# Kernel tuning notes

Measured on AMD Instinct MI355X. Metric: run time of the kernel, lower is better.

Reference implementation:

```python
import jax, jax.numpy as jnp
import numpy as np

B, N, S, K, D = 8, 16384, 1024, 32, 64
MLP = [64, 64, 128]
C_IN = 3 + D  # grouped_xyz_norm (3) concat grouped point features (D)
EPS = 1e-5


def setup_inputs() -> dict:
    key = jax.random.key(0)
    ks = jax.random.split(key, 16)
    inp = {
        "xyz": jax.random.normal(ks[0], (B, 3, N), dtype=jnp.float32),
        "points": jax.random.normal(ks[1], (B, D, N), dtype=jnp.float32),
        "sample_idx": jax.random.randint(ks[2], (B, S), 0, N, dtype=jnp.int32),
    }
    last = C_IN
    for i, oc in enumerate(MLP):
        scale = 1.0 / np.sqrt(last)
        inp[f"w{i}"] = jax.random.uniform(ks[3 + 4 * i], (oc, last), jnp.float32, -scale, scale)
        inp[f"b{i}"] = jax.random.uniform(ks[4 + 4 * i], (oc,), jnp.float32, -scale, scale)
        inp[f"g{i}"] = jnp.ones((oc,), jnp.float32)   # BN gamma
        inp[f"be{i}"] = jnp.zeros((oc,), jnp.float32)  # BN beta
        last = oc
    return inp


def _gather(pts, idx):
    # pts: [B,N,C], idx: [B,...] -> [B,...,C]
    return jax.vmap(lambda p, i: p[i])(pts, idx)


def _mlp_layer(x, w, b, g, be):
    # x: [B,C,K,S]; 1x1 Conv2d + BatchNorm2d (training-mode batch stats) + ReLU
    y = jnp.einsum("bcks,oc->boks", x, w) + b[None, :, None, None]
    mu = jnp.mean(y, axis=(0, 2, 3), keepdims=True)
    var = jnp.var(y, axis=(0, 2, 3), keepdims=True)
    y = (y - mu) * jax.lax.rsqrt(var + EPS)
    y = y * g[None, :, None, None] + be[None, :, None, None]
    return jax.nn.relu(y)


def reference(xyz, points, sample_idx, w0, b0, g0, be0, w1, b1, g1, be1, w2, b2, g2, be2):
    xyz_t = jnp.transpose(xyz, (0, 2, 1))      # [B,N,3]
    pts_t = jnp.transpose(points, (0, 2, 1))   # [B,N,D]
    idx_s = sample_idx.astype(jnp.int32)

    new_xyz = _gather(xyz_t, idx_s)            # [B,S,3]

    # square_distance(new_xyz, xyz): [B,S,N]
    d = (jnp.sum(new_xyz ** 2, -1)[:, :, None]
         + jnp.sum(xyz_t ** 2, -1)[:, None, :]
         - 2.0 * jnp.einsum("bsc,bnc->bsn", new_xyz, xyz_t))
    _, idx = jax.lax.top_k(-d, K)              # kNN indices [B,S,K]

    grouped_xyz = _gather(xyz_t, idx)          # [B,S,K,3]
    grouped_norm = grouped_xyz - new_xyz[:, :, None, :]
    grouped_pts = _gather(pts_t, idx)          # [B,S,K,D]
    feat = jnp.concatenate([grouped_norm, grouped_pts], axis=-1)  # [B,S,K,3+D]

    x = jnp.transpose(feat, (0, 3, 2, 1))      # [B,C,K,S]
    x = _mlp_layer(x, w0, b0, g0, be0)
    x = _mlp_layer(x, w1, b1, g1, be1)
    x = _mlp_layer(x, w2, b2, g2, be2)
    new_points = jnp.max(x, axis=2)            # [B,128,S]

    return (jnp.transpose(new_xyz, (0, 2, 1)), new_points, grouped_xyz, idx_s)
```

## Files before the change

### kernel.cpp

```cpp
#include <hip/hip_runtime.h>

constexpr int cB = 8, cN = 16384, cS = 1024, cK = 32, cD = 64;
constexpr int cO2 = 128;
constexpr int PTOT = cB * cS * cK;
constexpr int NBLK2 = PTOT / 128;

constexpr int OUT1_OFF = cB * 3 * cS;
constexpr int OUT2_OFF = OUT1_OFF + cB * cO2 * cS;
constexpr int OUT3_OFF = OUT2_OFF + cB * cS * cK * 3;

constexpr size_t WS_PTS  = 0;
constexpr size_t WS_XYZP = WS_PTS  + (size_t)cB * cN * cD * 4;
constexpr size_t WS_IDX  = WS_XYZP + (size_t)cB * cN * 16;
constexpr size_t WS_NORM = WS_IDX  + (size_t)PTOT * 4;
constexpr size_t WS_Y0   = WS_NORM + (size_t)PTOT * 3 * 4;
constexpr size_t WS_Y1   = WS_Y0   + (size_t)PTOT * 64 * 4;
constexpr size_t WS_MX   = WS_Y1   + (size_t)PTOT * 64 * 4;
constexpr size_t WS_MN   = WS_MX   + (size_t)cB * cS * cO2 * 4;
constexpr size_t WS_P0   = WS_MN   + (size_t)cB * cS * cO2 * 4;
constexpr size_t WS_P1   = WS_P0   + (size_t)NBLK2 * 64 * 2 * 8;
constexpr size_t WS_P2   = WS_P1   + (size_t)NBLK2 * 64 * 2 * 8;
constexpr size_t WS_BN   = WS_P2   + (size_t)NBLK2 * 128 * 2 * 8;
constexpr size_t WS_END  = WS_BN   + 3 * 128 * 2 * 4;

__device__ __forceinline__ unsigned keyOf(float d) {
    unsigned u = __float_as_uint(d);
    return u ^ ((unsigned)((int)u >> 31) | 0x80000000u);
}
__device__ __forceinline__ float distNp(float qx, float qy, float qz, float sq, float4 p) {
    float m0 = __fmul_rn(qx, p.x);
    float m1 = __fmul_rn(qy, p.y);
    float m2 = __fmul_rn(qz, p.z);
    float dt = __fadd_rn(__fadd_rn(m0, m1), m2);
    return __fsub_rn(__fadd_rn(sq, p.w), __fmul_rn(2.0f, dt));
}

__global__ __launch_bounds__(256) void k_prep(const float* __restrict__ pts,
                                              const float* __restrict__ xyz,
                                              float* __restrict__ ptsT,
                                              float4* __restrict__ xyzp) {
    __shared__ float tile[64][65];
    int blk = blockIdx.x;
    int tid = threadIdx.x;
    if (blk < 2048) {
        int b = blk >> 8;
        int n0 = (blk & 255) * 64;
        for (int it = 0; it < 16; ++it) {
            int l = it * 256 + tid;
            int c = l >> 6, nn = l & 63;
            tile[nn][c] = pts[((size_t)b * 64 + c) * cN + n0 + nn];
        }
        __syncthreads();
        for (int it = 0; it < 16; ++it) {
            int l = it * 256 + tid;
            int nn = l >> 6, c = l & 63;
            ptsT[((size_t)(b * cN + n0 + nn)) * 64 + c] = tile[nn][c];
        }
    } else {
        int i = (blk - 2048) * 256 + tid;
        int b = i >> 14, n = i & (cN - 1);
        float x = xyz[(b * 3 + 0) * cN + n];
        float y = xyz[(b * 3 + 1) * cN + n];
        float z = xyz[(b * 3 + 2) * cN + n];
        float sq = __fadd_rn(__fadd_rn(__fmul_rn(x, x), __fmul_rn(y, y)), __fmul_rn(z, z));
        xyzp[i] = make_float4(x, y, z, sq);
    }
}

#define QB 8
#define CAP2 192

__device__ __forceinline__ void selectBin2(const unsigned* __restrict__ h, int lane,
                                           int target, int* Tout, int* cbOut) {
    int base = lane * 8;
    unsigned hh[8];
    unsigned c8 = 0;
#pragma unroll
    for (int i = 0; i < 8; i++) { hh[i] = h[base + i]; c8 += hh[i]; }
    unsigned incl = c8;
#pragma unroll
    for (int off = 1; off < 32; off <<= 1) {
        unsigned t = __shfl_up(incl, (unsigned)off, 32);
        if (lane >= off) incl += t;
    }
    int excl = (int)(incl - c8);
    if (excl < target && target <= (int)incl) {
        int c = excl;
#pragma unroll
        for (int i = 0; i < 8; i++) {
            int nc = c + (int)hh[i];
            if (c < target && target <= nc) { *Tout = base + i; *cbOut = c; }
            c = nc;
        }
    }
}

__global__ __launch_bounds__(256, 4) void k_knn(const float* __restrict__ xyz,
                                                const int* __restrict__ sidx_g,
                                                const float4* __restrict__ xyzp,
                                                int* __restrict__ idxw,
                                                float* __restrict__ normw,
                                                float* __restrict__ outbuf) {
    __shared__ unsigned hist[QB][258];
    __shared__ unsigned long long wmask[QB][256];
    __shared__ unsigned long long cand2[QB][CAP2];
    __shared__ unsigned cnt2[QB];
    __shared__ float qxs[QB], qys[QB], qzs[QB], sqs[QB];
    __shared__ int sIdx[QB];
    __shared__ float s1s[QB], tAs[QB], tBs[QB];
    __shared__ int T1s[QB], cb1s[QB], T2s[QB], cb2s[QB];
    __shared__ float fTs[QB];
    __shared__ int nRf[QB];
    __shared__ int anyR;
    __shared__ unsigned order[QB][cK];

    int tid = threadIdx.x;
    int qi = tid >> 5, lane = tid & 31;
    int wid = tid >> 6;
    int qbase = blockIdx.x * QB;
    int b = qbase / cS;
    int s0 = qbase % cS;
    const float4* pb = xyzp + (size_t)b * cN;

    if (tid < QB) {
        int si = sidx_g[b * cS + s0 + tid];
        sIdx[tid] = si;
        float x = xyz[(b * 3 + 0) * cN + si];
        float y = xyz[(b * 3 + 1) * cN + si];
        float z = xyz[(b * 3 + 2) * cN + si];
        qxs[tid] = x; qys[tid] = y; qzs[tid] = z;
        sqs[tid] = __fadd_rn(__fadd_rn(__fmul_rn(x, x), __fmul_rn(y, y)), __fmul_rn(z, z));
        cnt2[tid] = 0u;
    }
    if (tid == 0) anyR = 0;
    for (int i = tid; i < QB * 258; i += 256) ((unsigned*)hist)[i] = 0u;
    __syncthreads();

    float qx = qxs[qi], qy = qys[qi], qz = qzs[qi], qsq = sqs[qi];

    {
        float dmin = 3.4e38f;
        for (int t = 0; t < 64; ++t) {
            float4 p = pb[lane + 32 * t];
            float dot = fmaf(qx, p.x, fmaf(qy, p.y, qz * p.z));
            float d = fmaf(-2.0f, dot, qsq + p.w);
            dmin = fminf(dmin, d);
        }
        float rmax = dmin;
#pragma unroll
        for (int off = 16; off; off >>= 1)
            rmax = fmaxf(rmax, __shfl_xor(rmax, off, 32));
        if (lane == 0) {
            float R = fmaxf(rmax, 1e-12f);
            float s1 = 254.0f / R;
            s1s[qi] = s1;
            tAs[qi] = qsq * s1;
            tBs[qi] = -2.0f * s1;
        }
    }
    __syncthreads();

    float lqx[QB], lqy[QB], lqz[QB], lS[QB], lA[QB], lB[QB];
#pragma unroll
    for (int q = 0; q < QB; q++) {
        lqx[q] = qxs[q]; lqy[q] = qys[q]; lqz[q] = qzs[q];
        lS[q] = s1s[q]; lA[q] = tAs[q]; lB[q] = tBs[q];
    }
    bool wlead = (tid & 63) == 0;

    for (int j = 0; j < cN / 256; ++j) {
        float4 p = pb[j * 256 + tid];
#pragma unroll
        for (int q = 0; q < QB; ++q) {
            float dot = fmaf(lqx[q], p.x, fmaf(lqy[q], p.y, lqz[q] * p.z));
            float t = fmaf(dot, lB[q], fmaf(p.w, lS[q], lA[q]));
            unsigned long long mk = __ballot(t < 258.0f);
            if (wlead) wmask[q][j * 4 + wid] = mk;
            if (t < 258.0f) {
                int bin = __float2int_rz(fmaxf(t, 0.0f));
                atomicAdd(&hist[q][bin], 1u);
            }
        }
    }
    __syncthreads();

    selectBin2(hist[qi], lane, cK, &T1s[qi], &cb1s[qi]);
    __syncthreads();
    if (tid < QB) {
        int T1 = T1s[tid];
        int acc = cb1s[tid] + (int)hist[tid][T1] + (int)hist[tid][T1 + 1];
        int nr = (acc > CAP2) ? 1 : 0;
        nRf[tid] = nr;
        fTs[tid] = (float)(T1 + 2);
        if (nr) atomicOr(&anyR, 1);
    }
    __syncthreads();

    if (anyR) {
        for (int i = tid; i < QB * 258; i += 256) ((unsigned*)hist)[i] = 0u;
        __syncthreads();
        if (nRf[qi]) {
            float fT1 = (float)T1s[qi];
            float tB = tBs[qi], tS = s1s[qi], tA = tAs[qi];
            for (int w = lane; w < 256; w += 32) {
                unsigned long long m = wmask[qi][w];
                int base = w * 64;
                while (m) {
                    int bit = (int)__ffsll((unsigned long long)m) - 1;
                    m &= m - 1;
                    float4 p = pb[base + bit];
                    float dot = fmaf(qx, p.x, fmaf(qy, p.y, qz * p.z));
                    float t = fmaf(dot, tB, fmaf(p.w, tS, tA));
                    float um = fmaxf(t, 0.0f) - fT1;
                    if (um >= 0.0f && um < 2.0f)
                        atomicAdd(&hist[qi][min(255, __float2int_rz(um * 128.0f))], 1u);
                }
            }
        }
        __syncthreads();
        if (nRf[qi]) selectBin2(hist[qi], lane, cK - cb1s[qi], &T2s[qi], &cb2s[qi]);
        __syncthreads();
        if (tid < QB && nRf[tid])
            fTs[tid] = (float)T1s[tid] + (float)(T2s[tid] + 2) * 0.0078125f;
        __syncthreads();
    }

    {
        float fT = fTs[qi];
        float tB = tBs[qi], tS = s1s[qi], tA = tAs[qi];
        for (int w = lane; w < 256; w += 32) {
            unsigned long long m = wmask[qi][w];
            int base = w * 64;
            while (m) {
                int bit = (int)__ffsll((unsigned long long)m) - 1;
                m &= m - 1;
                int n = base + bit;
                float4 p = pb[n];
                float dot = fmaf(qx, p.x, fmaf(qy, p.y, qz * p.z));
                float t = fmaf(dot, tB, fmaf(p.w, tS, tA));
                if (t < fT) {
                    float de = distNp(qx, qy, qz, qsq, p);
                    unsigned pos = atomicAdd(&cnt2[qi], 1u);
                    if (pos < CAP2)
                        cand2[qi][pos] = ((unsigned long long)keyOf(de) << 32) | (unsigned)n;
                }
            }
        }
    }
    __syncthreads();

    int m2 = (int)min(cnt2[qi], (unsigned)CAP2);
    for (int r = 0; r < cK; ++r) {
        unsigned long long best = ~0ull;
        int bslot = -1;
        for (int i = lane; i < m2; i += 32) {
            unsigned long long v = cand2[qi][i];
            if (v < best) { best = v; bslot = i; }
        }
#pragma unroll
        for (int off = 16; off; off >>= 1) {
            unsigned long long ov = __shfl_xor(best, off, 32);
            int os = __shfl_xor(bslot, off, 32);
            if (ov < best) { best = ov; bslot = os; }
        }
        if (lane == 0) {
            order[qi][r] = (best != ~0ull) ? (unsigned)(best & 0xFFFFFFFFull) : 0u;
            if (bslot >= 0) cand2[qi][bslot] = ~0ull;
        }
    }

    {
        int r = lane;
        int s = s0 + qi;
        int n = (int)order[qi][r];
        size_t pos = (size_t)(b * cS + s) * cK + r;
        idxw[pos] = n;
        float px = xyz[(b * 3 + 0) * cN + n];
        float py = xyz[(b * 3 + 1) * cN + n];
        float pz = xyz[(b * 3 + 2) * cN + n];
        outbuf[OUT2_OFF + pos * 3 + 0] = px;
        outbuf[OUT2_OFF + pos * 3 + 1] = py;
        outbuf[OUT2_OFF + pos * 3 + 2] = pz;
        normw[pos * 3 + 0] = __fsub_rn(px, qxs[qi]);
        normw[pos * 3 + 1] = __fsub_rn(py, qys[qi]);
        normw[pos * 3 + 2] = __fsub_rn(pz, qzs[qi]);
        if (r == 0) {
            outbuf[OUT3_OFF + b * cS + s] = (float)sIdx[qi];
            outbuf[(b * 3 + 0) * cS + s] = qxs[qi];
            outbuf[(b * 3 + 1) * cS + s] = qys[qi];
            outbuf[(b * 3 + 2) * cS + s] = qzs[qi];
        }
    }
}

__global__ __launch_bounds__(256) void k_conv0(const int* __restrict__ idxw,
                                               const float* __restrict__ normw,
                                               const float* __restrict__ ptsT,
                                               const float* __restrict__ w0,
                                               const float* __restrict__ b0,
                                               float* __restrict__ y0,
                                               double* __restrict__ part0) {
    __shared__ __align__(16) float fAT[67 * 132];
    __shared__ __align__(16) float wT[67 * 68];
    __shared__ float bl[64];
    int tid = threadIdx.x;
    int blk = blockIdx.x;
    int b = blk >> 8;
    int s0 = (blk & 255) << 2;
    size_t posbase = ((size_t)b * cS + s0) * cK;

    for (int l = tid; l < 64 * 67; l += 256) {
        int o = l / 67, c = l - o * 67;
        wT[c * 68 + o] = w0[l];
    }
    if (tid < 64) bl[tid] = b0[tid];
    {
        int r = tid >> 1, half = tid & 1;
        size_t pos = posbase + r;
        int n = idxw[pos];
        const float* pr = ptsT + ((size_t)b * cN + n) * 64 + half * 32;
#pragma unroll
        for (int q = 0; q < 8; q++) {
            float4 v = *(const float4*)(pr + q * 4);
            int c = 3 + half * 32 + q * 4;
            fAT[(c + 0) * 132 + r] = v.x;
            fAT[(c + 1) * 132 + r] = v.y;
            fAT[(c + 2) * 132 + r] = v.z;
            fAT[(c + 3) * 132 + r] = v.w;
        }
        if (half == 0) {
            fAT[0 * 132 + r] = normw[pos * 3 + 0];
            fAT[1 * 132 + r] = normw[pos * 3 + 1];
            fAT[2 * 132 + r] = normw[pos * 3 + 2];
        }
    }
    __syncthreads();

    int ry = tid >> 4, tx = tid & 15;
    float acc[8][4];
#pragma unroll
    for (int i = 0; i < 8; i++)
#pragma unroll
        for (int j = 0; j < 4; j++) acc[i][j] = bl[tx * 4 + j];

    for (int c = 0; c < 67; ++c) {
        const float* fb = fAT + c * 132;
        float4 a0 = *(const float4*)(fb + ry * 8);
        float4 a1 = *(const float4*)(fb + ry * 8 + 4);
        float4 wv = *(const float4*)&wT[c * 68 + tx * 4];
        float av[8] = {a0.x, a0.y, a0.z, a0.w, a1.x, a1.y, a1.z, a1.w};
#pragma unroll
        for (int i = 0; i < 8; i++) {
            acc[i][0] = fmaf(av[i], wv.x, acc[i][0]);
            acc[i][1] = fmaf(av[i], wv.y, acc[i][1]);
            acc[i][2] = fmaf(av[i], wv.z, acc[i][2]);
            acc[i][3] = fmaf(av[i], wv.w, acc[i][3]);
        }
    }
#pragma unroll
    for (int i = 0; i < 8; i++) {
        float4 o4 = make_float4(acc[i][0], acc[i][1], acc[i][2], acc[i][3]);
        *(float4*)(y0 + (posbase + ry * 8 + i) * 64 + tx * 4) = o4;
    }
    __syncthreads();

    float* ps = wT;
    float* pq = wT + 16 * 64;
#pragma unroll
    for (int j = 0; j < 4; j++) {
        float s = 0.f, q = 0.f;
#pragma unroll
        for (int i = 0; i < 8; i++) { float v = acc[i][j]; s += v; q += v * v; }
        ps[ry * 64 + tx * 4 + j] = s;
        pq[ry * 64 + tx * 4 + j] = q;
    }
    __syncthreads();
    if (tid < 64) {
        float s = 0.f, q = 0.f;
        for (int t = 0; t < 16; t++) { s += ps[t * 64 + tid]; q += pq[t * 64 + tid]; }
        part0[((size_t)blk * 64 + tid) * 2 + 0] = (double)s;
        part0[((size_t)blk * 64 + tid) * 2 + 1] = (double)q;
    }
}

__global__ __launch_bounds__(256) void k_conv1(const float* __restrict__ yin,
                                               const float2* __restrict__ bnin,
                                               const float* __restrict__ w,
                                               const float* __restrict__ bb,
                                               float* __restrict__ yout,
                                               double* __restrict__ part) {
    __shared__ __align__(16) float fAT[64 * 132];
    __shared__ __align__(16) float wT[64 * 68];
    __shared__ float bl[64], al[64], sl[64];
    int tid = threadIdx.x;
    int blk = blockIdx.x;
    int b = blk >> 8;
    int s0 = (blk & 255) << 2;
    size_t posbase = ((size_t)b * cS + s0) * cK;

    if (tid < 64) {
        bl[tid] = bb[tid];
        float2 t = bnin[tid];
        al[tid] = t.x; sl[tid] = t.y;
    }
    __syncthreads();
    for (int l = tid; l < 64 * 64; l += 256) {
        int o = l >> 6, c = l & 63;
        wT[c * 68 + o] = w[l];
    }
    {
        int r = tid >> 1, half = tid & 1;
        const float* yr = yin + (posbase + r) * 64 + half * 32;
#pragma unroll
        for (int q = 0; q < 8; q++) {
            float4 v = *(const float4*)(yr + q * 4);
            int c = half * 32 + q * 4;
            v.x = fmaxf(fmaf(v.x, al[c + 0], sl[c + 0]), 0.0f);
            v.y = fmaxf(fmaf(v.y, al[c + 1], sl[c + 1]), 0.0f);
            v.z = fmaxf(fmaf(v.z, al[c + 2], sl[c + 2]), 0.0f);
            v.w = fmaxf(fmaf(v.w, al[c + 3], sl[c + 3]), 0.0f);
            fAT[(c + 0) * 132 + r] = v.x;
            fAT[(c + 1) * 132 + r] = v.y;
            fAT[(c + 2) * 132 + r] = v.z;
            fAT[(c + 3) * 132 + r] = v.w;
        }
    }
    __syncthreads();

    int ry = tid >> 4, tx = tid & 15;
    float acc[8][4];
#pragma unroll
    for (int i = 0; i < 8; i++)
#pragma unroll
        for (int j = 0; j < 4; j++) acc[i][j] = bl[tx * 4 + j];

    for (int c = 0; c < 64; ++c) {
        const float* fb = fAT + c * 132;
        float4 a0 = *(const float4*)(fb + ry * 8);
        float4 a1 = *(const float4*)(fb + ry * 8 + 4);
        float4 wv = *(const float4*)&wT[c * 68 + tx * 4];
        float av[8] = {a0.x, a0.y, a0.z, a0.w, a1.x, a1.y, a1.z, a1.w};
#pragma unroll
        for (int i = 0; i < 8; i++) {
            acc[i][0] = fmaf(av[i], wv.x, acc[i][0]);
            acc[i][1] = fmaf(av[i], wv.y, acc[i][1]);
            acc[i][2] = fmaf(av[i], wv.z, acc[i][2]);
            acc[i][3] = fmaf(av[i], wv.w, acc[i][3]);
        }
    }
#pragma unroll
    for (int i = 0; i < 8; i++) {
        float4 o4 = make_float4(acc[i][0], acc[i][1], acc[i][2], acc[i][3]);
        *(float4*)(yout + (posbase + ry * 8 + i) * 64 + tx * 4) = o4;
    }
    __syncthreads();

    float* ps = wT;
    float* pq = wT + 16 * 64;
#pragma unroll
    for (int j = 0; j < 4; j++) {
        float s = 0.f, q = 0.f;
#pragma unroll
        for (int i = 0; i < 8; i++) { float v = acc[i][j]; s += v; q += v * v; }
        ps[ry * 64 + tx * 4 + j] = s;
        pq[ry * 64 + tx * 4 + j] = q;
    }
    __syncthreads();
    if (tid < 64) {
        float s = 0.f, q = 0.f;
        for (int t = 0; t < 16; t++) { s += ps[t * 64 + tid]; q += pq[t * 64 + tid]; }
        part[((size_t)blk * 64 + tid) * 2 + 0] = (double)s;
        part[((size_t)blk * 64 + tid) * 2 + 1] = (double)q;
    }
}

__global__ __launch_bounds__(256) void k_conv2(const float* __restrict__ y1,
                                               const float2* __restrict__ bn1,
                                               const float* __restrict__ w2,
                                               const float* __restrict__ b2,
                                               float* __restrict__ mx,
                                               float* __restrict__ mn,
                                               double* __restrict__ part2) {
    __shared__ __align__(16) float fAT[64 * 132];
    __shared__ __align__(16) float wT[64 * 132];
    __shared__ float al[64], sl[64], bl[128];
    int tid = threadIdx.x;
    int blk = blockIdx.x;
    int b = blk >> 8;
    int s0 = (blk & 255) << 2;
    size_t posbase = ((size_t)b * cS + s0) * cK;

    if (tid < 64) { float2 t = bn1[tid]; al[tid] = t.x; sl[tid] = t.y; }
    if (tid < 128) bl[tid] = b2[tid];
    __syncthreads();

    {
        int r = tid >> 1, half = tid & 1;
        const float* yr = y1 + (posbase + r) * 64 + half * 32;
#pragma unroll
        for (int q = 0; q < 8; q++) {
            float4 v = *(const float4*)(yr + q * 4);
            int c = half * 32 + q * 4;
            v.x = fmaxf(fmaf(v.x, al[c + 0], sl[c + 0]), 0.0f);
            v.y = fmaxf(fmaf(v.y, al[c + 1], sl[c + 1]), 0.0f);
            v.z = fmaxf(fmaf(v.z, al[c + 2], sl[c + 2]), 0.0f);
            v.w = fmaxf(fmaf(v.w, al[c + 3], sl[c + 3]), 0.0f);
            fAT[(c + 0) * 132 + r] = v.x;
            fAT[(c + 1) * 132 + r] = v.y;
            fAT[(c + 2) * 132 + r] = v.z;
            fAT[(c + 3) * 132 + r] = v.w;
        }
    }
    for (int l = tid; l < 128 * 64; l += 256) {
        int o = l >> 6, c = l & 63;
        wT[c * 132 + o] = w2[l];
    }
    __syncthreads();

    int ry = tid >> 4, tx = tid & 15;
    float acc[8][8];
#pragma unroll
    for (int i = 0; i < 8; i++) {
#pragma unroll
        for (int j = 0; j < 4; j++) acc[i][j] = bl[tx * 4 + j];
#pragma unroll
        for (int j = 4; j < 8; j++) acc[i][j] = bl[64 + tx * 4 + (j - 4)];
    }

    for (int c = 0; c < 64; ++c) {
        const float* fb = fAT + c * 132;
        const float* wb = wT + c * 132;
        float4 a0 = *(const float4*)(fb + ry * 8);
        float4 a1 = *(const float4*)(fb + ry * 8 + 4);
        float4 w0v = *(const float4*)(wb + tx * 4);
        float4 w1v = *(const float4*)(wb + 64 + tx * 4);
        float av[8] = {a0.x, a0.y, a0.z, a0.w, a1.x, a1.y, a1.z, a1.w};
        float wv[8] = {w0v.x, w0v.y, w0v.z, w0v.w, w1v.x, w1v.y, w1v.z, w1v.w};
#pragma unroll
        for (int i = 0; i < 8; i++)
#pragma unroll
            for (int j = 0; j < 8; j++)
                acc[i][j] = fmaf(av[i], wv[j], acc[i][j]);
    }
    __syncthreads();

    float* ps  = wT;
    float* pq  = wT + 16 * 128;
    float* pmx = wT + 32 * 128;
    float* pmn = wT + 48 * 128;
#pragma unroll
    for (int j = 0; j < 8; j++) {
        int o = (j < 4) ? (tx * 4 + j) : (64 + tx * 4 + (j - 4));
        float s = 0.f, q = 0.f;
        float mv = -3.402823466e+38f, nv = 3.402823466e+38f;
#pragma unroll
        for (int i = 0; i < 8; i++) {
            float v = acc[i][j];
            s += v; q += v * v;
            mv = fmaxf(mv, v); nv = fminf(nv, v);
        }
        ps[ry * 128 + o] = s;
        pq[ry * 128 + o] = q;
        pmx[ry * 128 + o] = mv;
        pmn[ry * 128 + o] = nv;
    }
    __syncthreads();
    if (tid < 128) {
        float s = 0.f, q = 0.f;
        for (int t = 0; t < 16; t++) { s += ps[t * 128 + tid]; q += pq[t * 128 + tid]; }
        part2[((size_t)blk * 128 + tid) * 2 + 0] = (double)s;
        part2[((size_t)blk * 128 + tid) * 2 + 1] = (double)q;
    }
    for (int e = tid; e < 512; e += 256) {
        int sg = e >> 7, o = e & 127;
        float mv = -3.402823466e+38f, nv = 3.402823466e+38f;
        for (int t = sg * 4; t < sg * 4 + 4; ++t) {
            mv = fmaxf(mv, pmx[t * 128 + o]);
            nv = fminf(nv, pmn[t * 128 + o]);
        }
        int s = s0 + sg;
        mx[((size_t)b * cS + s) * 128 + o] = mv;
        mn[((size_t)b * cS + s) * 128 + o] = nv;
    }
}

__global__ __launch_bounds__(256) void k_fin(const double* __restrict__ part, int nblk,
                                             int oc,
                                             const float* __restrict__ g,
                                             const float* __restrict__ be,
                                             float2* __restrict__ bnout) {
    __shared__ double rs[256], rq[256];
    int o = blockIdx.x;
    int tid = threadIdx.x;
    double s = 0.0, q = 0.0;
    for (int i = tid; i < nblk; i += 256) {
        const double* p = part + ((size_t)i * oc + o) * 2;
        s += p[0];
        q += p[1];
    }
    rs[tid] = s; rq[tid] = q;
    __syncthreads();
    for (int off = 128; off; off >>= 1) {
        if (tid < off) { rs[tid] += rs[tid + off]; rq[tid] += rq[tid + off]; }
        __syncthreads();
    }
    if (tid == 0) {
        double cntv = (double)PTOT;
        double mu = rs[0] / cntv;
        double var = rq[0] / cntv - mu * mu;
        if (var < 0.0) var = 0.0;
        float a = (float)((double)g[o] / sqrt(var + 1e-5));
        float sh = (float)((double)be[o] - mu * (double)a);
        bnout[o] = make_float2(a, sh);
    }
}

__global__ __launch_bounds__(256) void k_final(const float* __restrict__ mx,
                                               const float* __restrict__ mn,
                                               const float2* __restrict__ bn2,
                                               float* __restrict__ out1) {
    int i = blockIdx.x * 256 + threadIdx.x;
    int b = i >> 17;
    int r = i & ((1 << 17) - 1);
    int o = r >> 10;
    int s = r & 1023;
    float2 t = bn2[o];
    size_t idx = ((size_t)b * cS + s) * 128 + o;
    float M = (t.x >= 0.0f) ? mx[idx] : mn[idx];
    out1[i] = fmaxf(t.x * M + t.y, 0.0f);
}

extern "C" void kernel_launch(void* const* d_in, const int* in_sizes, int n_in,
                              void* d_out, int out_size, void* d_ws, size_t ws_size,
                              hipStream_t stream) {
    (void)in_sizes; (void)n_in; (void)out_size;
    const float* xyz = (const float*)d_in[0];
    const float* pts = (const float*)d_in[1];
    const int* sidx  = (const int*)d_in[2];
    const float* w0  = (const float*)d_in[3];
    const float* b0  = (const float*)d_in[4];
    const float* g0  = (const float*)d_in[5];
    const float* be0 = (const float*)d_in[6];
    const float* w1  = (const float*)d_in[7];
    const float* b1  = (const float*)d_in[8];
    const float* g1  = (const float*)d_in[9];
    const float* be1 = (const float*)d_in[10];
    const float* w2  = (const float*)d_in[11];
    const float* b2  = (const float*)d_in[12];
    const float* g2  = (const float*)d_in[13];
    const float* be2 = (const float*)d_in[14];
    float* out = (float*)d_out;
    char* ws = (char*)d_ws;
    if (ws_size < WS_END) return;

    float* ptsT  = (float*)(ws + WS_PTS);
    float4* xyzp = (float4*)(ws + WS_XYZP);
    int* idxw    = (int*)(ws + WS_IDX);
    float* normw = (float*)(ws + WS_NORM);
    float* y0    = (float*)(ws + WS_Y0);
    float* y1    = (float*)(ws + WS_Y1);
    float* mx    = (float*)(ws + WS_MX);
    float* mn    = (float*)(ws + WS_MN);
    double* p0   = (double*)(ws + WS_P0);
    double* p1   = (double*)(ws + WS_P1);
    double* p2   = (double*)(ws + WS_P2);
    float2* bnb  = (float2*)(ws + WS_BN);

    hipLaunchKernelGGL(k_prep, dim3(2048 + cB * cN / 256), dim3(256), 0, stream,
                       pts, xyz, ptsT, xyzp);
    hipLaunchKernelGGL(k_knn, dim3(cB * cS / QB), dim3(256), 0, stream,
                       xyz, sidx, xyzp, idxw, normw, out);
    hipLaunchKernelGGL(k_conv0, dim3(NBLK2), dim3(256), 0, stream,
                       idxw, normw, ptsT, w0, b0, y0, p0);
    hipLaunchKernelGGL(k_fin, dim3(64), dim3(256), 0, stream, p0, NBLK2, 64, g0, be0, bnb);
    hipLaunchKernelGGL(k_conv1, dim3(NBLK2), dim3(256), 0, stream, y0, bnb, w1, b1, y1, p1);
    hipLaunchKernelGGL(k_fin, dim3(64), dim3(256), 0, stream, p1, NBLK2, 64, g1, be1, bnb + 128);
    hipLaunchKernelGGL(k_conv2, dim3(NBLK2), dim3(256), 0, stream,
                       y1, bnb + 128, w2, b2, mx, mn, p2);
    hipLaunchKernelGGL(k_fin, dim3(128), dim3(256), 0, stream, p2, NBLK2, 128, g2, be2, bnb + 256);
    hipLaunchKernelGGL(k_final, dim3(cB * cO2 * cS / 256), dim3(256), 0, stream,
                       mx, mn, bnb + 256, out + OUT1_OFF);
}
```

Measured before the change: 395.9 us.

## Bin points into a 2D spatial grid and scan only nearby cells in kNN

Adds counting, scan and scatter kernels that sort the points of each batch into a 32x32 grid over (z,y) and reorder the queries along a serpentine cell order, so the eight queries in a block are spatially close. The kNN kernel then computes a bounding window of cells from each query's radius estimate and runs its histogram, refine and candidate passes only over points in those cells, instead of the full 16K points and the wavefront ballot masks. This cuts distance work and drops the wmask shared buffer. In exchange it adds several small launches and atomics, and it relies on the fixed grid range of ±4.5, beyond which coordinates are clamped into the edge cells.

```diff
diff --git a/kernel.cpp b/kernel.cpp
--- a/kernel.cpp
+++ b/kernel.cpp
@@ -4,6 +4,11 @@
 constexpr int cO2 = 128;
 constexpr int PTOT = cB * cS * cK;
 constexpr int NBLK2 = PTOT / 128;
+
+constexpr int GR = 32;
+constexpr int GC2 = GR * GR;
+#define GL 4.5f
+#define GINV (32.0f / 9.0f)
 
 constexpr int OUT1_OFF = cB * 3 * cS;
 constexpr int OUT2_OFF = OUT1_OFF + cB * cO2 * cS;
@@ -23,6 +28,13 @@
 constexpr size_t WS_BN   = WS_P2   + (size_t)NBLK2 * 128 * 2 * 8;
 constexpr size_t WS_END  = WS_BN   + 3 * 128 * 2 * 4;
 
+constexpr size_t WS_SPT  = WS_Y0;
+constexpr size_t WS_SIX  = WS_SPT + (size_t)cB * cN * 16;
+constexpr size_t WS_PCNT = WS_SIX + (size_t)cB * cN * 4;
+constexpr size_t WS_QCNT = WS_PCNT + (size_t)cB * GC2 * 4;
+constexpr size_t WS_PCS  = WS_QCNT + (size_t)cB * GC2 * 4;
+constexpr size_t WS_QORD = WS_PCS + (size_t)cB * (GC2 + 1) * 4;
+
 __device__ __forceinline__ unsigned keyOf(float d) {
     unsigned u = __float_as_uint(d);
     return u ^ ((unsigned)((int)u >> 31) | 0x80000000u);
@@ -33,6 +45,18 @@
     float m2 = __fmul_rn(qz, p.z);
     float dt = __fadd_rn(__fadd_rn(m0, m1), m2);
     return __fsub_rn(__fadd_rn(sq, p.w), __fmul_rn(2.0f, dt));
+}
+
+__device__ __forceinline__ int cellClamp(float v) {
+    return min(GR - 1, max(0, (int)floorf((v + GL) * GINV)));
+}
+__device__ __forceinline__ int pcell(float4 p) {
+    return cellClamp(p.z) * GR + cellClamp(p.y);
+}
+__device__ __forceinline__ int qkey(float qy, float qz) {
+    int cy = cellClamp(qy), cz = cellClamp(qz);
+    int yy = (cz & 1) ? (GR - 1 - cy) : cy;
+    return cz * GR + yy;
 }
 
 __global__ __launch_bounds__(256) void k_prep(const float* __restrict__ pts,
@@ -67,6 +91,82 @@
     }
 }
 
+__global__ __launch_bounds__(256) void k_cnt(const float4* __restrict__ xyzp,
+                                             const float* __restrict__ xyz,
+                                             const int* __restrict__ sidx_g,
+                                             int* __restrict__ pcnt,
+                                             int* __restrict__ qcnt) {
+    int blk = blockIdx.x, tid = threadIdx.x;
+    if (blk < 512) {
+        int i = blk * 256 + tid;
+        int b = i >> 14;
+        atomicAdd(&pcnt[b * GC2 + pcell(xyzp[i])], 1);
+    } else {
+        int i = (blk - 512) * 256 + tid;
+        int b = i >> 10, s = i & (cS - 1);
+        int si = sidx_g[b * cS + s];
+        float qy = xyz[(b * 3 + 1) * cN + si];
+        float qz = xyz[(b * 3 + 2) * cN + si];
+        atomicAdd(&qcnt[b * GC2 + qkey(qy, qz)], 1);
+    }
+}
+
+__global__ __launch_bounds__(256) void k_scan(int* __restrict__ pcnt,
+                                              int* __restrict__ qcnt,
+                                              int* __restrict__ pcs) {
+    __shared__ int s[256];
+    int b = blockIdx.x >> 1, kind = blockIdx.x & 1;
+    int tid = threadIdx.x;
+    int* cnt = (kind == 0) ? (pcnt + b * GC2) : (qcnt + b * GC2);
+    const int CBC = GC2 / 256;
+    int base = tid * CBC;
+    int sum = 0;
+    for (int k = 0; k < CBC; ++k) sum += cnt[base + k];
+    s[tid] = sum;
+    __syncthreads();
+    for (int off = 1; off < 256; off <<= 1) {
+        int v = (tid >= off) ? s[tid - off] : 0;
+        __syncthreads();
+        s[tid] += v;
+        __syncthreads();
+    }
+    int run = s[tid] - sum;
+    for (int k = 0; k < CBC; ++k) {
+        int v = cnt[base + k];
+        if (kind == 0) pcs[(size_t)b * (GC2 + 1) + base + k] = run;
+        cnt[base + k] = run;
+        run += v;
+    }
+    if (kind == 0 && tid == 255) pcs[(size_t)b * (GC2 + 1) + GC2] = run;
+}
+
+__global__ __launch_bounds__(256) void k_scat(const float4* __restrict__ xyzp,
+                                              const float* __restrict__ xyz,
+                                              const int* __restrict__ sidx_g,
+                                              int* __restrict__ pcnt,
+                                              int* __restrict__ qcnt,
+                                              float4* __restrict__ spt,
+                                              int* __restrict__ six,
+                                              int* __restrict__ qord) {
+    int blk = blockIdx.x, tid = threadIdx.x;
+    if (blk < 512) {
+        int i = blk * 256 + tid;
+        int b = i >> 14, n = i & (cN - 1);
+        float4 p = xyzp[i];
+        int pos = atomicAdd(&pcnt[b * GC2 + pcell(p)], 1);
+        spt[(size_t)b * cN + pos] = p;
+        six[(size_t)b * cN + pos] = n;
+    } else {
+        int i = (blk - 512) * 256 + tid;
+        int b = i >> 10, s = i & (cS - 1);
+        int si = sidx_g[b * cS + s];
+        float qy = xyz[(b * 3 + 1) * cN + si];
+        float qz = xyz[(b * 3 + 2) * cN + si];
+        int pos = atomicAdd(&qcnt[b * GC2 + qkey(qy, qz)], 1);
+        qord[b * cS + pos] = s;
+    }
+}
+
 #define QB 8
 #define CAP2 192
 
@@ -98,32 +198,41 @@
 __global__ __launch_bounds__(256, 4) void k_knn(const float* __restrict__ xyz,
                                                 const int* __restrict__ sidx_g,
                                                 const float4* __restrict__ xyzp,
+                                                const float4* __restrict__ spt,
+                                                const int* __restrict__ six,
+                                                const int* __restrict__ pcs,
+                                                const int* __restrict__ qord,
                                                 int* __restrict__ idxw,
                                                 float* __restrict__ normw,
                                                 float* __restrict__ outbuf) {
     __shared__ unsigned hist[QB][258];
-    __shared__ unsigned long long wmask[QB][256];
     __shared__ unsigned long long cand2[QB][CAP2];
     __shared__ unsigned cnt2[QB];
     __shared__ float qxs[QB], qys[QB], qzs[QB], sqs[QB];
-    __shared__ int sIdx[QB];
+    __shared__ int sIdx[QB], sQ[QB];
     __shared__ float s1s[QB], tAs[QB], tBs[QB];
     __shared__ int T1s[QB], cb1s[QB], T2s[QB], cb2s[QB];
     __shared__ float fTs[QB];
     __shared__ int nRf[QB];
     __shared__ int anyR;
+    __shared__ int wzl, wzh, wyl, wyh;
     __shared__ unsigned order[QB][cK];
 
     int tid = threadIdx.x;
     int qi = tid >> 5, lane = tid & 31;
-    int wid = tid >> 6;
     int qbase = blockIdx.x * QB;
     int b = qbase / cS;
     int s0 = qbase % cS;
     const float4* pb = xyzp + (size_t)b * cN;
-
+    const float4* sp = spt + (size_t)b * cN;
+    const int* sx = six + (size_t)b * cN;
+    const int* CSb = pcs + (size_t)b * (GC2 + 1);
+
+    if (tid == 0) { anyR = 0; wzl = GR; wzh = -1; wyl = GR; wyh = -1; }
     if (tid < QB) {
-        int si = sidx_g[b * cS + s0 + tid];
+        int sq = qord[b * cS + s0 + tid];
+        sQ[tid] = sq;
+        int si = sidx_g[b * cS + sq];
         sIdx[tid] = si;
         float x = xyz[(b * 3 + 0) * cN + si];
         float y = xyz[(b * 3 + 1) * cN + si];
@@ -132,7 +241,6 @@
         sqs[tid] = __fadd_rn(__fadd_rn(__fmul_rn(x, x), __fmul_rn(y, y)), __fmul_rn(z, z));
         cnt2[tid] = 0u;
     }
-    if (tid == 0) anyR = 0;
     for (int i = tid; i < QB * 258; i += 256) ((unsigned*)hist)[i] = 0u;
     __syncthreads();
 
@@ -156,6 +264,13 @@
             s1s[qi] = s1;
             tAs[qi] = qsq * s1;
             tBs[qi] = -2.0f * s1;
+            float rq = sqrtf(R * 1.001f);
+            int zlo = max(0, (int)floorf((qz - rq + GL) * GINV));
+            int zhi = min(GR - 1, (int)floorf((qz + rq + GL) * GINV));
+            int ylo = max(0, (int)floorf((qy - rq + GL) * GINV));
+            int yhi = min(GR - 1, (int)floorf((qy + rq + GL) * GINV));
+            atomicMin(&wzl, zlo); atomicMax(&wzh, zhi);
+            atomicMin(&wyl, ylo); atomicMax(&wyh, yhi);
         }
     }
     __syncthreads();
@@ -166,19 +281,20 @@
         lqx[q] = qxs[q]; lqy[q] = qys[q]; lqz[q] = qzs[q];
         lS[q] = s1s[q]; lA[q] = tAs[q]; lB[q] = tBs[q];
     }
-    bool wlead = (tid & 63) == 0;
-
-    for (int j = 0; j < cN / 256; ++j) {
-        float4 p = pb[j * 256 + tid];
-#pragma unroll
-        for (int q = 0; q < QB; ++q) {
-            float dot = fmaf(lqx[q], p.x, fmaf(lqy[q], p.y, lqz[q] * p.z));
-            float t = fmaf(dot, lB[q], fmaf(p.w, lS[q], lA[q]));
-            unsigned long long mk = __ballot(t < 258.0f);
-            if (wlead) wmask[q][j * 4 + wid] = mk;
-            if (t < 258.0f) {
-                int bin = __float2int_rz(fmaxf(t, 0.0f));
-                atomicAdd(&hist[q][bin], 1u);
+    int zl = wzl, zh = wzh, yl = wyl, yh = wyh;
+
+    for (int cz = zl; cz <= zh; ++cz) {
+        int st = CSb[cz * GR + yl], en = CSb[cz * GR + yh + 1];
+        for (int i = st + tid; i < en; i += 256) {
+            float4 p = sp[i];
+#pragma unroll
+            for (int q = 0; q < QB; ++q) {
+                float dot = fmaf(lqx[q], p.x, fmaf(lqy[q], p.y, lqz[q] * p.z));
+                float t = fmaf(dot, lB[q], fmaf(p.w, lS[q], lA[q]));
+                if (t < 258.0f) {
+                    int bin = __float2int_rz(fmaxf(t, 0.0f));
+                    atomicAdd(&hist[q][bin], 1u);
+                }
             }
         }
     }
@@ -199,21 +315,22 @@
     if (anyR) {
         for (int i = tid; i < QB * 258; i += 256) ((unsigned*)hist)[i] = 0u;
         __syncthreads();
-        if (nRf[qi]) {
-            float fT1 = (float)T1s[qi];
-            float tB = tBs[qi], tS = s1s[qi], tA = tAs[qi];
-            for (int w = lane; w < 256; w += 32) {
-                unsigned long long m = wmask[qi][w];
-                int base = w * 64;
-                while (m) {
-                    int bit = (int)__ffsll((unsigned long long)m) - 1;
-                    m &= m - 1;
-                    float4 p = pb[base + bit];
-                    float dot = fmaf(qx, p.x, fmaf(qy, p.y, qz * p.z));
-                    float t = fmaf(dot, tB, fmaf(p.w, tS, tA));
-                    float um = fmaxf(t, 0.0f) - fT1;
-                    if (um >= 0.0f && um < 2.0f)
-                        atomicAdd(&hist[qi][min(255, __float2int_rz(um * 128.0f))], 1u);
+        int lT1[QB], go[QB];
+#pragma unroll
+        for (int q = 0; q < QB; q++) { lT1[q] = T1s[q]; go[q] = nRf[q]; }
+        for (int cz = zl; cz <= zh; ++cz) {
+            int st = CSb[cz * GR + yl], en = CSb[cz * GR + yh + 1];
+            for (int i = st + tid; i < en; i += 256) {
+                float4 p = sp[i];
+#pragma unroll
+                for (int q = 0; q < QB; ++q) {
+                    if (go[q]) {
+                        float dot = fmaf(lqx[q], p.x, fmaf(lqy[q], p.y, lqz[q] * p.z));
+                        float t = fmaf(dot, lB[q], fmaf(p.w, lS[q], lA[q]));
+                        float um = fmaxf(t, 0.0f) - (float)lT1[q];
+                        if (um >= 0.0f && um < 2.0f)
+                            atomicAdd(&hist[q][min(255, __float2int_rz(um * 128.0f))], 1u);
+                    }
                 }
             }
         }
@@ -225,24 +342,24 @@
         __syncthreads();
     }
 
-    {
-        float fT = fTs[qi];
-        float tB = tBs[qi], tS = s1s[qi], tA = tAs[qi];
-        for (int w = lane; w < 256; w += 32) {
-            unsigned long long m = wmask[qi][w];
-            int base = w * 64;
-            while (m) {
-                int bit = (int)__ffsll((unsigned long long)m) - 1;
-                m &= m - 1;
-                int n = base + bit;
-                float4 p = pb[n];
-                float dot = fmaf(qx, p.x, fmaf(qy, p.y, qz * p.z));
-                float t = fmaf(dot, tB, fmaf(p.w, tS, tA));
-                if (t < fT) {
-                    float de = distNp(qx, qy, qz, qsq, p);
-                    unsigned pos = atomicAdd(&cnt2[qi], 1u);
+    float lsq[QB], lt[QB];
+#pragma unroll
+    for (int q = 0; q < QB; q++) { lsq[q] = sqs[q]; lt[q] = fTs[q]; }
+
+    for (int cz = zl; cz <= zh; ++cz) {
+        int st = CSb[cz * GR + yl], en = CSb[cz * GR + yh + 1];
+        for (int i = st + tid; i < en; i += 256) {
+            float4 p = sp[i];
+#pragma unroll
+            for (int q = 0; q < QB; ++q) {
+                float dot = fmaf(lqx[q], p.x, fmaf(lqy[q], p.y, lqz[q] * p.z));
+                float t = fmaf(dot, lB[q], fmaf(p.w, lS[q], lA[q]));
+                if (t < lt[q]) {
+                    float de = distNp(lqx[q], lqy[q], lqz[q], lsq[q], p);
+                    int n = sx[i];
+                    unsigned pos = atomicAdd(&cnt2[q], 1u);
                     if (pos < CAP2)
-                        cand2[qi][pos] = ((unsigned long long)keyOf(de) << 32) | (unsigned)n;
+                        cand2[q][pos] = ((unsigned long long)keyOf(de) << 32) | (unsigned)n;
                 }
             }
         }
@@ -271,7 +388,7 @@
 
     {
         int r = lane;
-        int s = s0 + qi;
+        int s = sQ[qi];
         int n = (int)order[qi][r];
         size_t pos = (size_t)(b * cS + s) * cK + r;
         idxw[pos] = n;
@@ -665,11 +782,23 @@
     double* p1   = (double*)(ws + WS_P1);
     double* p2   = (double*)(ws + WS_P2);
     float2* bnb  = (float2*)(ws + WS_BN);
+    float4* spt  = (float4*)(ws + WS_SPT);
+    int* six     = (int*)(ws + WS_SIX);
+    int* pcnt    = (int*)(ws + WS_PCNT);
+    int* qcnt    = (int*)(ws + WS_QCNT);
+    int* pcs     = (int*)(ws + WS_PCS);
+    int* qord    = (int*)(ws + WS_QORD);
 
     hipLaunchKernelGGL(k_prep, dim3(2048 + cB * cN / 256), dim3(256), 0, stream,
                        pts, xyz, ptsT, xyzp);
+    hipMemsetAsync(ws + WS_PCNT, 0, (size_t)cB * GC2 * 4 * 2, stream);
+    hipLaunchKernelGGL(k_cnt, dim3(512 + 32), dim3(256), 0, stream,
+                       xyzp, xyz, sidx, pcnt, qcnt);
+    hipLaunchKernelGGL(k_scan, dim3(2 * cB), dim3(256), 0, stream, pcnt, qcnt, pcs);
+    hipLaunchKernelGGL(k_scat, dim3(512 + 32), dim3(256), 0, stream,
+                       xyzp, xyz, sidx, pcnt, qcnt, spt, six, qord);
     hipLaunchKernelGGL(k_knn, dim3(cB * cS / QB), dim3(256), 0, stream,
-                       xyz, sidx, xyzp, idxw, normw, out);
+                       xyz, sidx, xyzp, spt, six, pcs, qord, idxw, normw, out);
     hipLaunchKernelGGL(k_conv0, dim3(NBLK2), dim3(256), 0, stream,
                        idxw, normw, ptsT, w0, b0, y0, p0);
     hipLaunchKernelGGL(k_fin, dim3(64), dim3(256), 0, stream, p0, NBLK2, 64, g0, be0, bnb);
```

New measurement: 419.5 us. 1.06x slower.

## Replace ballot-mask candidate compaction in kNN with full rescans; store BN partials as float2

Applied to the files above, without the earlier changes.

The kNN kernel no longer records per-wave ballot masks of points under the histogram threshold. The refinement histogram and candidate collection passes now rescan all N points for every query. This removes the 16KB wmask shared array and the per-iteration ballots, and raises the candidate capacity to 256. In exchange it repeats distance evaluation over every point, and it halves the BN partial-sum traffic by storing float pairs instead of doubles, at some precision risk in the per-block sums.

```diff
diff --git a/kernel.cpp b/kernel.cpp
--- a/kernel.cpp
+++ b/kernel.cpp
@@ -18,9 +18,9 @@
 constexpr size_t WS_MX   = WS_Y1   + (size_t)PTOT * 64 * 4;
 constexpr size_t WS_MN   = WS_MX   + (size_t)cB * cS * cO2 * 4;
 constexpr size_t WS_P0   = WS_MN   + (size_t)cB * cS * cO2 * 4;
-constexpr size_t WS_P1   = WS_P0   + (size_t)NBLK2 * 64 * 2 * 8;
-constexpr size_t WS_P2   = WS_P1   + (size_t)NBLK2 * 64 * 2 * 8;
-constexpr size_t WS_BN   = WS_P2   + (size_t)NBLK2 * 128 * 2 * 8;
+constexpr size_t WS_P1   = WS_P0   + (size_t)NBLK2 * 64 * 8;
+constexpr size_t WS_P2   = WS_P1   + (size_t)NBLK2 * 64 * 8;
+constexpr size_t WS_BN   = WS_P2   + (size_t)NBLK2 * 128 * 8;
 constexpr size_t WS_END  = WS_BN   + 3 * 128 * 2 * 4;
 
 __device__ __forceinline__ unsigned keyOf(float d) {
@@ -68,7 +68,7 @@
 }
 
 #define QB 8
-#define CAP2 192
+#define CAP 256
 
 __device__ __forceinline__ void selectBin2(const unsigned* __restrict__ h, int lane,
                                            int target, int* Tout, int* cbOut) {
@@ -102,21 +102,19 @@
                                                 float* __restrict__ normw,
                                                 float* __restrict__ outbuf) {
     __shared__ unsigned hist[QB][258];
-    __shared__ unsigned long long wmask[QB][256];
-    __shared__ unsigned long long cand2[QB][CAP2];
-    __shared__ unsigned cnt2[QB];
+    __shared__ unsigned long long cand[QB][CAP];
+    __shared__ unsigned cnt[QB];
     __shared__ float qxs[QB], qys[QB], qzs[QB], sqs[QB];
     __shared__ int sIdx[QB];
     __shared__ float s1s[QB], tAs[QB], tBs[QB];
     __shared__ int T1s[QB], cb1s[QB], T2s[QB], cb2s[QB];
-    __shared__ float fTs[QB];
-    __shared__ int nRf[QB];
-    __shared__ int anyR;
+    __shared__ float tAcc[QB];
+    __shared__ int refq[QB];
+    __shared__ int anyRef;
     __shared__ unsigned order[QB][cK];
 
     int tid = threadIdx.x;
     int qi = tid >> 5, lane = tid & 31;
-    int wid = tid >> 6;
     int qbase = blockIdx.x * QB;
     int b = qbase / cS;
     int s0 = qbase % cS;
@@ -130,15 +128,14 @@
         float z = xyz[(b * 3 + 2) * cN + si];
         qxs[tid] = x; qys[tid] = y; qzs[tid] = z;
         sqs[tid] = __fadd_rn(__fadd_rn(__fmul_rn(x, x), __fmul_rn(y, y)), __fmul_rn(z, z));
-        cnt2[tid] = 0u;
-    }
-    if (tid == 0) anyR = 0;
+        cnt[tid] = 0u;
+    }
+    if (tid == 0) anyRef = 0;
     for (int i = tid; i < QB * 258; i += 256) ((unsigned*)hist)[i] = 0u;
     __syncthreads();
 
-    float qx = qxs[qi], qy = qys[qi], qz = qzs[qi], qsq = sqs[qi];
-
     {
+        float qx = qxs[qi], qy = qys[qi], qz = qzs[qi], qsq = sqs[qi];
         float dmin = 3.4e38f;
         for (int t = 0; t < 64; ++t) {
             float4 p = pb[lane + 32 * t];
@@ -166,7 +163,6 @@
         lqx[q] = qxs[q]; lqy[q] = qys[q]; lqz[q] = qzs[q];
         lS[q] = s1s[q]; lA[q] = tAs[q]; lB[q] = tBs[q];
     }
-    bool wlead = (tid & 63) == 0;
 
     for (int j = 0; j < cN / 256; ++j) {
         float4 p = pb[j * 256 + tid];
@@ -174,8 +170,6 @@
         for (int q = 0; q < QB; ++q) {
             float dot = fmaf(lqx[q], p.x, fmaf(lqy[q], p.y, lqz[q] * p.z));
             float t = fmaf(dot, lB[q], fmaf(p.w, lS[q], lA[q]));
-            unsigned long long mk = __ballot(t < 258.0f);
-            if (wlead) wmask[q][j * 4 + wid] = mk;
             if (t < 258.0f) {
                 int bin = __float2int_rz(fmaxf(t, 0.0f));
                 atomicAdd(&hist[q][bin], 1u);
@@ -189,72 +183,69 @@
     if (tid < QB) {
         int T1 = T1s[tid];
         int acc = cb1s[tid] + (int)hist[tid][T1] + (int)hist[tid][T1 + 1];
-        int nr = (acc > CAP2) ? 1 : 0;
-        nRf[tid] = nr;
-        fTs[tid] = (float)(T1 + 2);
-        if (nr) atomicOr(&anyR, 1);
-    }
-    __syncthreads();
-
-    if (anyR) {
+        int nr = (acc > CAP) ? 1 : 0;
+        refq[tid] = nr;
+        tAcc[tid] = (float)(T1 + 2);
+        if (nr) atomicOr(&anyRef, 1);
+    }
+    __syncthreads();
+
+    if (anyRef) {
         for (int i = tid; i < QB * 258; i += 256) ((unsigned*)hist)[i] = 0u;
         __syncthreads();
-        if (nRf[qi]) {
-            float fT1 = (float)T1s[qi];
-            float tB = tBs[qi], tS = s1s[qi], tA = tAs[qi];
-            for (int w = lane; w < 256; w += 32) {
-                unsigned long long m = wmask[qi][w];
-                int base = w * 64;
-                while (m) {
-                    int bit = (int)__ffsll((unsigned long long)m) - 1;
-                    m &= m - 1;
-                    float4 p = pb[base + bit];
-                    float dot = fmaf(qx, p.x, fmaf(qy, p.y, qz * p.z));
-                    float t = fmaf(dot, tB, fmaf(p.w, tS, tA));
-                    float um = fmaxf(t, 0.0f) - fT1;
-                    if (um >= 0.0f && um < 2.0f)
-                        atomicAdd(&hist[qi][min(255, __float2int_rz(um * 128.0f))], 1u);
+        int lT1[QB], lrf[QB];
+#pragma unroll
+        for (int q = 0; q < QB; q++) { lT1[q] = T1s[q]; lrf[q] = refq[q]; }
+        for (int j = 0; j < cN / 256; ++j) {
+            float4 p = pb[j * 256 + tid];
+#pragma unroll
+            for (int q = 0; q < QB; ++q) {
+                if (lrf[q]) {
+                    float dot = fmaf(lqx[q], p.x, fmaf(lqy[q], p.y, lqz[q] * p.z));
+                    float t = fmaf(dot, lB[q], fmaf(p.w, lS[q], lA[q]));
+                    float um = fmaxf(t, 0.0f) - (float)lT1[q];
+                    if (um >= 0.0f && um < 2.0f) {
+                        int sub = min(255, __float2int_rz(um * 128.0f));
+                        atomicAdd(&hist[q][sub], 1u);
+                    }
                 }
             }
         }
         __syncthreads();
-        if (nRf[qi]) selectBin2(hist[qi], lane, cK - cb1s[qi], &T2s[qi], &cb2s[qi]);
+        if (refq[qi]) selectBin2(hist[qi], lane, cK - cb1s[qi], &T2s[qi], &cb2s[qi]);
         __syncthreads();
-        if (tid < QB && nRf[tid])
-            fTs[tid] = (float)T1s[tid] + (float)(T2s[tid] + 2) * 0.0078125f;
+        if (tid < QB && refq[tid])
+            tAcc[tid] = (float)T1s[tid] + (float)(T2s[tid] + 2) * 0.0078125f;
         __syncthreads();
     }
 
-    {
-        float fT = fTs[qi];
-        float tB = tBs[qi], tS = s1s[qi], tA = tAs[qi];
-        for (int w = lane; w < 256; w += 32) {
-            unsigned long long m = wmask[qi][w];
-            int base = w * 64;
-            while (m) {
-                int bit = (int)__ffsll((unsigned long long)m) - 1;
-                m &= m - 1;
-                int n = base + bit;
-                float4 p = pb[n];
-                float dot = fmaf(qx, p.x, fmaf(qy, p.y, qz * p.z));
-                float t = fmaf(dot, tB, fmaf(p.w, tS, tA));
-                if (t < fT) {
-                    float de = distNp(qx, qy, qz, qsq, p);
-                    unsigned pos = atomicAdd(&cnt2[qi], 1u);
-                    if (pos < CAP2)
-                        cand2[qi][pos] = ((unsigned long long)keyOf(de) << 32) | (unsigned)n;
-                }
+    float lsq[QB], lt[QB];
+#pragma unroll
+    for (int q = 0; q < QB; q++) { lsq[q] = sqs[q]; lt[q] = tAcc[q]; }
+
+    for (int j = 0; j < cN / 256; ++j) {
+        int n = j * 256 + tid;
+        float4 p = pb[n];
+#pragma unroll
+        for (int q = 0; q < QB; ++q) {
+            float dot = fmaf(lqx[q], p.x, fmaf(lqy[q], p.y, lqz[q] * p.z));
+            float t = fmaf(dot, lB[q], fmaf(p.w, lS[q], lA[q]));
+            if (t < lt[q]) {
+                float de = distNp(lqx[q], lqy[q], lqz[q], lsq[q], p);
+                unsigned pos = atomicAdd(&cnt[q], 1u);
+                if (pos < CAP)
+                    cand[q][pos] = ((unsigned long long)keyOf(de) << 32) | (unsigned)n;
             }
         }
     }
     __syncthreads();
 
-    int m2 = (int)min(cnt2[qi], (unsigned)CAP2);
+    int m = (int)min(cnt[qi], (unsigned)CAP);
     for (int r = 0; r < cK; ++r) {
         unsigned long long best = ~0ull;
         int bslot = -1;
-        for (int i = lane; i < m2; i += 32) {
-            unsigned long long v = cand2[qi][i];
+        for (int i = lane; i < m; i += 32) {
+            unsigned long long v = cand[qi][i];
             if (v < best) { best = v; bslot = i; }
         }
 #pragma unroll
@@ -265,7 +256,7 @@
         }
         if (lane == 0) {
             order[qi][r] = (best != ~0ull) ? (unsigned)(best & 0xFFFFFFFFull) : 0u;
-            if (bslot >= 0) cand2[qi][bslot] = ~0ull;
+            if (bslot >= 0) cand[qi][bslot] = ~0ull;
         }
     }
 
@@ -299,7 +290,7 @@
                                                const float* __restrict__ w0,
                                                const float* __restrict__ b0,
                                                float* __restrict__ y0,
-                                               double* __restrict__ part0) {
+                                               float2* __restrict__ part0) {
     __shared__ __align__(16) float fAT[67 * 132];
     __shared__ __align__(16) float wT[67 * 68];
     __shared__ float bl[64];
@@ -378,8 +369,7 @@
     if (tid < 64) {
         float s = 0.f, q = 0.f;
         for (int t = 0; t < 16; t++) { s += ps[t * 64 + tid]; q += pq[t * 64 + tid]; }
-        part0[((size_t)blk * 64 + tid) * 2 + 0] = (double)s;
-        part0[((size_t)blk * 64 + tid) * 2 + 1] = (double)q;
+        part0[(size_t)blk * 64 + tid] = make_float2(s, q);
     }
 }
 
@@ -388,7 +378,7 @@
                                                const float* __restrict__ w,
                                                const float* __restrict__ bb,
                                                float* __restrict__ yout,
-                                               double* __restrict__ part) {
+                                               float2* __restrict__ part) {
     __shared__ __align__(16) float fAT[64 * 132];
     __shared__ __align__(16) float wT[64 * 68];
     __shared__ float bl[64], al[64], sl[64];
@@ -469,8 +459,7 @@
     if (tid < 64) {
         float s = 0.f, q = 0.f;
         for (int t = 0; t < 16; t++) { s += ps[t * 64 + tid]; q += pq[t * 64 + tid]; }
-        part[((size_t)blk * 64 + tid) * 2 + 0] = (double)s;
-        part[((size_t)blk * 64 + tid) * 2 + 1] = (double)q;
+        part[(size_t)blk * 64 + tid] = make_float2(s, q);
     }
 }
 
@@ -480,7 +469,7 @@
                                                const float* __restrict__ b2,
                                                float* __restrict__ mx,
                                                float* __restrict__ mn,
-                                               double* __restrict__ part2) {
+                                               float2* __restrict__ part2) {
     __shared__ __align__(16) float fAT[64 * 132];
     __shared__ __align__(16) float wT[64 * 132];
     __shared__ float al[64], sl[64], bl[128];
@@ -568,8 +557,7 @@
     if (tid < 128) {
         float s = 0.f, q = 0.f;
         for (int t = 0; t < 16; t++) { s += ps[t * 128 + tid]; q += pq[t * 128 + tid]; }
-        part2[((size_t)blk * 128 + tid) * 2 + 0] = (double)s;
-        part2[((size_t)blk * 128 + tid) * 2 + 1] = (double)q;
+        part2[(size_t)blk * 128 + tid] = make_float2(s, q);
     }
     for (int e = tid; e < 512; e += 256) {
         int sg = e >> 7, o = e & 127;
@@ -584,7 +572,7 @@
     }
 }
 
-__global__ __launch_bounds__(256) void k_fin(const double* __restrict__ part, int nblk,
+__global__ __launch_bounds__(256) void k_fin(const float2* __restrict__ part, int nblk,
                                              int oc,
                                              const float* __restrict__ g,
                                              const float* __restrict__ be,
@@ -594,9 +582,9 @@
     int tid = threadIdx.x;
     double s = 0.0, q = 0.0;
     for (int i = tid; i < nblk; i += 256) {
-        const double* p = part + ((size_t)i * oc + o) * 2;
-        s += p[0];
-        q += p[1];
+        float2 p = part[(size_t)i * oc + o];
+        s += (double)p.x;
+        q += (double)p.y;
     }
     rs[tid] = s; rq[tid] = q;
     __syncthreads();
@@ -661,9 +649,9 @@
     float* y1    = (float*)(ws + WS_Y1);
     float* mx    = (float*)(ws + WS_MX);
     float* mn    = (float*)(ws + WS_MN);
-    double* p0   = (double*)(ws + WS_P0);
-    double* p1   = (double*)(ws + WS_P1);
-    double* p2   = (double*)(ws + WS_P2);
+    float2* p0   = (float2*)(ws + WS_P0);
+    float2* p1   = (float2*)(ws + WS_P1);
+    float2* p2   = (float2*)(ws + WS_P2);
     float2* bnb  = (float2*)(ws + WS_BN);
 
     hipLaunchKernelGGL(k_prep, dim3(2048 + cB * cN / 256), dim3(256), 0, stream,
```

New measurement: 380.4 us, median of 2. -3.9%, faster.
